# Kernel tuning notes

Hardware: AMD Instinct MI355X
Metric: run time of the kernel (lower is better)

## Reference

```python
import jax, jax.numpy as jnp
import numpy as np

NEG_SLOPE = 0.2
EPS = 1e-16


def _add_self_loops(edge_index, num_nodes):
    loop = jnp.arange(num_nodes, dtype=edge_index.dtype)
    return jnp.concatenate([edge_index, jnp.stack([loop, loop])], axis=1)


def gat_conv(x, edge_index, W, a_src, a_dst, b, concat):
    """PyG-style GATConv: gather -> attention logits -> segment softmax -> scatter-add."""
    N = x.shape[0]
    H, C = a_src.shape
    xl = (x @ W).reshape(N, H, C)                       # [N,H,C]
    alpha_src = (xl * a_src[None]).sum(-1)              # [N,H]
    alpha_dst = (xl * a_dst[None]).sum(-1)              # [N,H]
    src, dst = edge_index[0], edge_index[1]
    alpha = jax.nn.leaky_relu(alpha_src[src] + alpha_dst[dst], NEG_SLOPE)  # [E,H]
    amax = jax.ops.segment_max(alpha, dst, num_segments=N)
    amax = jnp.where(jnp.isfinite(amax), amax, 0.0)
    ea = jnp.exp(alpha - amax[dst])
    denom = jax.ops.segment_sum(ea, dst, num_segments=N)
    attn = ea / (denom[dst] + EPS)                      # [E,H]
    msg = xl[src] * attn[:, :, None]                    # [E,H,C]
    out = jax.ops.segment_sum(msg, dst, num_segments=N)  # [N,H,C]
    out = out.reshape(N, H * C) if concat else out.mean(axis=1)
    return out + b


def setup_inputs() -> dict:
    key = jax.random.key(0)
    ks = jax.random.split(key, 9)
    N, F, E, H, C, NC = 100000, 128, 1600000, 8, 8, 40
    s = lambda fan: 1.0 / np.sqrt(fan)
    return {
        "x": jax.random.normal(ks[0], (N, F), dtype=jnp.float32),
        "edge_index": jax.random.randint(ks[1], (2, E), 0, N, dtype=jnp.int64),
        "W1": jax.random.normal(ks[2], (F, H * C), dtype=jnp.float32) * s(F),
        "a_src1": jax.random.normal(ks[3], (H, C), dtype=jnp.float32) * s(C),
        "a_dst1": jax.random.normal(ks[4], (H, C), dtype=jnp.float32) * s(C),
        "b1": jnp.zeros((H * C,), dtype=jnp.float32),
        "W2": jax.random.normal(ks[5], (H * C, NC), dtype=jnp.float32) * s(H * C),
        "a_src2": jax.random.normal(ks[6], (1, NC), dtype=jnp.float32) * s(NC),
        "a_dst2": jax.random.normal(ks[7], (1, NC), dtype=jnp.float32) * s(NC),
        "b2": jnp.zeros((NC,), dtype=jnp.float32),
    }


def reference(x, edge_index, W1, a_src1, a_dst1, b1, W2, a_src2, a_dst2, b2):
    N = x.shape[0]
    ei = _add_self_loops(edge_index, N)
    h = gat_conv(x, ei, W1, a_src1, a_dst1, b1, concat=True)   # [N,64]
    h = jax.nn.elu(h)
    out = gat_conv(h, ei, W2, a_src2, a_dst2, b2, concat=True)  # [N,nclass]
    return out
```

## Files before the change

kernel.cpp:

```cpp
#include <hip/hip_runtime.h>
#include <math.h>

#define NEG_SLOPE 0.2f
#define GAT_EPS 1e-16f
#define LOG2E 1.44269504088896340736f

#define CH   8192
#define NBK  256

__device__ __forceinline__ unsigned pack_bf16(float a, float b) {
    unsigned ua = __float_as_uint(a);
    unsigned ub = __float_as_uint(b);
    ua = (ua + 0x8000u) >> 16;
    ub = (ub + 0x8000u) & 0xffff0000u;
    return ua | ub;
}
__device__ __forceinline__ float bf_lo(unsigned pk) {
    return __uint_as_float(pk << 16);
}
__device__ __forceinline__ float bf_hi(unsigned pk) {
    return __uint_as_float(pk & 0xffff0000u);
}


__global__ __launch_bounds__(256) void k_cnt(
    const int* __restrict__ ei, int E, int N, int shift,
    int* __restrict__ cnt)
{
    __shared__ int h[NBK];
    int c = blockIdx.x;
    h[threadIdx.x] = 0;
    __syncthreads();
    int Etot = E + N;
    int base = c * CH;
    int lim = min(base + CH, Etot);
    for (int e = base + threadIdx.x; e < lim; e += 256) {
        int d = (e < E) ? ei[E + e] : (e - E);
        atomicAdd(&h[d >> shift], 1);
    }
    __syncthreads();
    cnt[c * NBK + threadIdx.x] = h[threadIdx.x];
}

__global__ __launch_bounds__(256) void k_off_a(
    const int* __restrict__ cnt, int* __restrict__ off,
    int* __restrict__ tot, int NCH)
{
    __shared__ int sm[256];
    int b = blockIdx.x;
    int t = threadIdx.x;
    int carry = 0;
    for (int c0 = 0; c0 < NCH; c0 += 256) {
        int c = c0 + t;
        int v = (c < NCH) ? cnt[c * NBK + b] : 0;
        sm[t] = v;
        __syncthreads();
        for (int o = 1; o < 256; o <<= 1) {
            int add = (t >= o) ? sm[t - o] : 0;
            __syncthreads();
            sm[t] += add;
            __syncthreads();
        }
        if (c < NCH) off[c * NBK + b] = carry + sm[t] - v;
        carry += sm[255];
        __syncthreads();
    }
    if (t == 0) tot[b] = carry;
}

__global__ __launch_bounds__(256) void k_off_b(
    const int* __restrict__ tot, int* __restrict__ bbase)
{
    __shared__ int sm[NBK];
    int b = threadIdx.x;
    int v0 = tot[b];
    sm[b] = v0;
    __syncthreads();
    for (int o = 1; o < NBK; o <<= 1) {
        int v = (b >= o) ? sm[b - o] : 0;
        __syncthreads();
        sm[b] += v;
        __syncthreads();
    }
    bbase[b] = sm[b] - v0;
    if (b == NBK - 1) bbase[NBK] = sm[b];
}

__global__ __launch_bounds__(256) void k_place(
    const int* __restrict__ ei, int E, int N, int shift,
    const int* __restrict__ off, const int* __restrict__ bbase,
    unsigned* __restrict__ bslab)
{
    __shared__ int cur[NBK];
    int c = blockIdx.x;
    cur[threadIdx.x] = bbase[threadIdx.x] + off[c * NBK + threadIdx.x];
    __syncthreads();
    int Etot = E + N;
    int base = c * CH;
    int lim = min(base + CH, Etot);
    int mask = (1 << shift) - 1;
    for (int e = base + threadIdx.x; e < lim; e += 256) {
        int s, d;
        if (e < E) { s = ei[e]; d = ei[E + e]; }
        else       { s = e - E; d = s; }
        int b = d >> shift;
        int pos = atomicAdd(&cur[b], 1);
        bslab[pos] = (unsigned)s | ((unsigned)(d & mask) << 17);
    }
}

__global__ __launch_bounds__(256) void k_csr2(
    const int* __restrict__ bbase, const unsigned* __restrict__ bslab,
    int shift, int* __restrict__ row_ptr, int* __restrict__ csr_src,
    int N, int Etot)
{
    __shared__ int sdeg[1024];
    __shared__ int scur[1024];
    __shared__ int ps[256];
    int b = blockIdx.x;
    int tid = threadIdx.x;
    int beg = bbase[b], end = bbase[b + 1];
    int nodes = 1 << shift;
    int node0 = b << shift;
    for (int i = tid; i < nodes; i += 256) sdeg[i] = 0;
    __syncthreads();
    for (int i = beg + tid; i < end; i += 256)
        atomicAdd(&sdeg[bslab[i] >> 17], 1);
    __syncthreads();
    int per = (nodes + 255) / 256;
    int mybase = tid * per;
    int sum = 0;
    for (int j = 0; j < per; j++) sum += sdeg[mybase + j];
    ps[tid] = sum;
    __syncthreads();
    int v0 = ps[tid];
    for (int o = 1; o < 256; o <<= 1) {
        int v = (tid >= o) ? ps[tid - o] : 0;
        __syncthreads();
        ps[tid] += v;
        __syncthreads();
    }
    int run = ps[tid] - v0;
    for (int j = 0; j < per; j++) {
        int i = mybase + j;
        int dgi = sdeg[i];
        scur[i] = beg + run;
        int node = node0 + i;
        if (node < N) row_ptr[node] = beg + run;
        run += dgi;
    }
    if (b == 0 && tid == 0) row_ptr[N] = Etot;
    __syncthreads();
    for (int i = beg + tid; i < end; i += 256) {
        unsigned w = bslab[i];
        int pos = atomicAdd(&scur[w >> 17], 1);
        csr_src[pos] = (int)(w & 0x1FFFFu);
    }
}

__global__ __launch_bounds__(256) void k_gemm1(
    const float* __restrict__ x, const float* __restrict__ W1,
    const float* __restrict__ a_src1, const float* __restrict__ a_dst1,
    unsigned* __restrict__ xl1b, float* __restrict__ as1,
    float* __restrict__ ad1, int N, int F)
{
    __shared__ float Ws[128 * 64];
    __shared__ float asrc[64];
    __shared__ float adst[64];
    for (int i = threadIdx.x; i < F * 64; i += 256) Ws[i] = W1[i];
    if (threadIdx.x < 64) {
        asrc[threadIdx.x] = a_src1[threadIdx.x];
        adst[threadIdx.x] = a_dst1[threadIdx.x];
    }
    __syncthreads();

    int n = blockIdx.x * 64 + (threadIdx.x >> 2);
    int q = threadIdx.x & 3;
    if (n >= N) return;
    int c0 = q * 16;

    float acc[16];
#pragma unroll
    for (int c = 0; c < 16; c++) acc[c] = 0.0f;

    const float4* xr4 = (const float4*)(x + (size_t)n * F);
    for (int k4 = 0; k4 < F / 4; k4++) {
        float4 xv = xr4[k4];
        const float* w0 = &Ws[(k4 * 4 + 0) * 64 + c0];
        const float* w1 = &Ws[(k4 * 4 + 1) * 64 + c0];
        const float* w2 = &Ws[(k4 * 4 + 2) * 64 + c0];
        const float* w3 = &Ws[(k4 * 4 + 3) * 64 + c0];
#pragma unroll
        for (int c = 0; c < 16; c++) {
            float a = acc[c];
            a = fmaf(xv.x, w0[c], a);
            a = fmaf(xv.y, w1[c], a);
            a = fmaf(xv.z, w2[c], a);
            a = fmaf(xv.w, w3[c], a);
            acc[c] = a;
        }
    }

    uint4 pk0, pk1;
    pk0.x = pack_bf16(acc[0], acc[1]);  pk0.y = pack_bf16(acc[2], acc[3]);
    pk0.z = pack_bf16(acc[4], acc[5]);  pk0.w = pack_bf16(acc[6], acc[7]);
    pk1.x = pack_bf16(acc[8], acc[9]);  pk1.y = pack_bf16(acc[10], acc[11]);
    pk1.z = pack_bf16(acc[12], acc[13]); pk1.w = pack_bf16(acc[14], acc[15]);
    uint4* xo = (uint4*)(xl1b + (size_t)n * 32 + q * 8);
    xo[0] = pk0;
    xo[1] = pk1;

#pragma unroll
    for (int hh = 0; hh < 2; hh++) {
        float s = 0.0f, t = 0.0f;
#pragma unroll
        for (int c = 0; c < 8; c++) {
            s = fmaf(acc[hh * 8 + c], asrc[c0 + hh * 8 + c], s);
            t = fmaf(acc[hh * 8 + c], adst[c0 + hh * 8 + c], t);
        }
        as1[(size_t)n * 8 + 2 * q + hh] = s * LOG2E;
        ad1[(size_t)n * 8 + 2 * q + hh] = t * LOG2E;
    }
}

__global__ __launch_bounds__(256) void k_agg1(
    const int* __restrict__ row_ptr, const int* __restrict__ csr_src,
    const float* __restrict__ as1, const float* __restrict__ ad1,
    const unsigned* __restrict__ xl1b, const float* __restrict__ b1,
    float* __restrict__ h1, int N)
{
    int d = blockIdx.x * 8 + ((threadIdx.x >> 6) << 1) + ((threadIdx.x >> 5) & 1);
    if (d >= N) return;
    int lane = threadIdx.x & 31;
    int g = lane >> 3;
    int l = lane & 7;

    int beg = row_ptr[d], end = row_ptr[d + 1];
    float adh = ad1[(size_t)d * 8 + l];

    float ax[8];
#pragma unroll
    for (int j = 0; j < 8; j++) ax[j] = 0.f;
    float den = 0.f;

    int i = beg + g;
    for (; i + 4 < end; i += 8) {
        int s0 = csr_src[i];
        int s1 = csr_src[i + 4];
        size_t q0 = (size_t)s0 * 8 + l;
        size_t q1 = (size_t)s1 * 8 + l;
        float al0 = as1[q0] + adh;
        float al1 = as1[q1] + adh;
        uint4 k0 = *(const uint4*)(xl1b + (q0 << 2));
        uint4 k1 = *(const uint4*)(xl1b + (q1 << 2));
        al0 = fmaxf(al0, NEG_SLOPE * al0);
        al1 = fmaxf(al1, NEG_SLOPE * al1);
        float e0 = __builtin_amdgcn_exp2f(al0);
        float e1 = __builtin_amdgcn_exp2f(al1);
        ax[0] = fmaf(e0, bf_lo(k0.x), ax[0]);
        ax[1] = fmaf(e0, bf_hi(k0.x), ax[1]);
        ax[2] = fmaf(e0, bf_lo(k0.y), ax[2]);
        ax[3] = fmaf(e0, bf_hi(k0.y), ax[3]);
        ax[4] = fmaf(e0, bf_lo(k0.z), ax[4]);
        ax[5] = fmaf(e0, bf_hi(k0.z), ax[5]);
        ax[6] = fmaf(e0, bf_lo(k0.w), ax[6]);
        ax[7] = fmaf(e0, bf_hi(k0.w), ax[7]);
        ax[0] = fmaf(e1, bf_lo(k1.x), ax[0]);
        ax[1] = fmaf(e1, bf_hi(k1.x), ax[1]);
        ax[2] = fmaf(e1, bf_lo(k1.y), ax[2]);
        ax[3] = fmaf(e1, bf_hi(k1.y), ax[3]);
        ax[4] = fmaf(e1, bf_lo(k1.z), ax[4]);
        ax[5] = fmaf(e1, bf_hi(k1.z), ax[5]);
        ax[6] = fmaf(e1, bf_lo(k1.w), ax[6]);
        ax[7] = fmaf(e1, bf_hi(k1.w), ax[7]);
        den += e0 + e1;
    }
    if (i < end) {
        int s0 = csr_src[i];
        size_t q0 = (size_t)s0 * 8 + l;
        float al0 = as1[q0] + adh;
        uint4 k0 = *(const uint4*)(xl1b + (q0 << 2));
        al0 = fmaxf(al0, NEG_SLOPE * al0);
        float e0 = __builtin_amdgcn_exp2f(al0);
        ax[0] = fmaf(e0, bf_lo(k0.x), ax[0]);
        ax[1] = fmaf(e0, bf_hi(k0.x), ax[1]);
        ax[2] = fmaf(e0, bf_lo(k0.y), ax[2]);
        ax[3] = fmaf(e0, bf_hi(k0.y), ax[3]);
        ax[4] = fmaf(e0, bf_lo(k0.z), ax[4]);
        ax[5] = fmaf(e0, bf_hi(k0.z), ax[5]);
        ax[6] = fmaf(e0, bf_lo(k0.w), ax[6]);
        ax[7] = fmaf(e0, bf_hi(k0.w), ax[7]);
        den += e0;
    }

#pragma unroll
    for (int m = 8; m < 32; m <<= 1) {
#pragma unroll
        for (int j = 0; j < 8; j++) ax[j] += __shfl_xor(ax[j], m);
        den += __shfl_xor(den, m);
    }

    if (g == 0) {
        float inv = __builtin_amdgcn_rcpf(den + GAT_EPS);
        const float4* bb = (const float4*)(b1 + l * 8);
        float4 b0 = bb[0], b1v = bb[1];
        float4 o0, o1;
        float v;
        v = fmaf(ax[0], inv, b0.x);  o0.x = v > 0.f ? v : __expf(v) - 1.f;
        v = fmaf(ax[1], inv, b0.y);  o0.y = v > 0.f ? v : __expf(v) - 1.f;
        v = fmaf(ax[2], inv, b0.z);  o0.z = v > 0.f ? v : __expf(v) - 1.f;
        v = fmaf(ax[3], inv, b0.w);  o0.w = v > 0.f ? v : __expf(v) - 1.f;
        v = fmaf(ax[4], inv, b1v.x); o1.x = v > 0.f ? v : __expf(v) - 1.f;
        v = fmaf(ax[5], inv, b1v.y); o1.y = v > 0.f ? v : __expf(v) - 1.f;
        v = fmaf(ax[6], inv, b1v.z); o1.z = v > 0.f ? v : __expf(v) - 1.f;
        v = fmaf(ax[7], inv, b1v.w); o1.w = v > 0.f ? v : __expf(v) - 1.f;
        float4* op = (float4*)(h1 + (size_t)d * 64 + l * 8);
        op[0] = o0;
        op[1] = o1;
    }
}

__global__ __launch_bounds__(256) void k_node2(
    const float* __restrict__ h1, const float* __restrict__ W2,
    const float* __restrict__ a_src2, const float* __restrict__ a_dst2,
    unsigned* __restrict__ xl2b, float* __restrict__ as2,
    float* __restrict__ ad2, int N)
{
    __shared__ float Ws[64 * 40];
    __shared__ float a2s[40];
    __shared__ float a2d[40];
    for (int i = threadIdx.x; i < 64 * 40; i += 256) Ws[i] = W2[i];
    if (threadIdx.x < 40) {
        a2s[threadIdx.x] = a_src2[threadIdx.x];
        a2d[threadIdx.x] = a_dst2[threadIdx.x];
    }
    __syncthreads();

    int n = blockIdx.x * 128 + (threadIdx.x >> 1);
    int q = threadIdx.x & 1;
    if (n >= N) return;
    int c0 = q * 20;

    float o[20];
#pragma unroll
    for (int j = 0; j < 20; j++) o[j] = 0.0f;

    const float4* hr4 = (const float4*)(h1 + (size_t)n * 64);
    for (int k4 = 0; k4 < 16; k4++) {
        float4 hv = hr4[k4];
        const float* w0 = &Ws[(k4 * 4 + 0) * 40 + c0];
        const float* w1 = &Ws[(k4 * 4 + 1) * 40 + c0];
        const float* w2 = &Ws[(k4 * 4 + 2) * 40 + c0];
        const float* w3 = &Ws[(k4 * 4 + 3) * 40 + c0];
#pragma unroll
        for (int j = 0; j < 20; j++) {
            float a = o[j];
            a = fmaf(hv.x, w0[j], a);
            a = fmaf(hv.y, w1[j], a);
            a = fmaf(hv.z, w2[j], a);
            a = fmaf(hv.w, w3[j], a);
            o[j] = a;
        }
    }

    float s = 0.0f, t = 0.0f;
#pragma unroll
    for (int j = 0; j < 20; j++) {
        s = fmaf(o[j], a2s[c0 + j], s);
        t = fmaf(o[j], a2d[c0 + j], t);
    }
    s += __shfl_xor(s, 1);
    t += __shfl_xor(t, 1);
    if (q == 0) { as2[n] = s * LOG2E; ad2[n] = t * LOG2E; }

    unsigned* xo = xl2b + (size_t)n * 20 + q * 10;
#pragma unroll
    for (int p = 0; p < 10; p++) xo[p] = pack_bf16(o[2 * p], o[2 * p + 1]);
}

__global__ __launch_bounds__(256) void k_agg2(
    const int* __restrict__ row_ptr, const int* __restrict__ csr_src,
    const float* __restrict__ as2, const float* __restrict__ ad2,
    const unsigned* __restrict__ xl2b, const float* __restrict__ b2,
    float* __restrict__ out, int N)
{
    int d = blockIdx.x * 8 + ((threadIdx.x >> 6) << 1) + ((threadIdx.x >> 5) & 1);
    if (d >= N) return;
    int lane = threadIdx.x & 31;
    int g = lane >> 3;
    int l = lane & 7;
    if (l >= 5) return;

    int beg = row_ptr[d], end = row_ptr[d + 1];
    float add = ad2[d];

    float ax[8];
#pragma unroll
    for (int j = 0; j < 8; j++) ax[j] = 0.f;
    float den = 0.f;

    int i = beg + g;
    for (; i + 4 < end; i += 8) {
        int s0 = csr_src[i];
        int s1 = csr_src[i + 4];
        float al0 = as2[s0] + add;
        float al1 = as2[s1] + add;
        uint4 k0 = *(const uint4*)(xl2b + (size_t)s0 * 20 + l * 4);
        uint4 k1 = *(const uint4*)(xl2b + (size_t)s1 * 20 + l * 4);
        al0 = fmaxf(al0, NEG_SLOPE * al0);
        al1 = fmaxf(al1, NEG_SLOPE * al1);
        float e0 = __builtin_amdgcn_exp2f(al0);
        float e1 = __builtin_amdgcn_exp2f(al1);
        ax[0] = fmaf(e0, bf_lo(k0.x), ax[0]);
        ax[1] = fmaf(e0, bf_hi(k0.x), ax[1]);
        ax[2] = fmaf(e0, bf_lo(k0.y), ax[2]);
        ax[3] = fmaf(e0, bf_hi(k0.y), ax[3]);
        ax[4] = fmaf(e0, bf_lo(k0.z), ax[4]);
        ax[5] = fmaf(e0, bf_hi(k0.z), ax[5]);
        ax[6] = fmaf(e0, bf_lo(k0.w), ax[6]);
        ax[7] = fmaf(e0, bf_hi(k0.w), ax[7]);
        ax[0] = fmaf(e1, bf_lo(k1.x), ax[0]);
        ax[1] = fmaf(e1, bf_hi(k1.x), ax[1]);
        ax[2] = fmaf(e1, bf_lo(k1.y), ax[2]);
        ax[3] = fmaf(e1, bf_hi(k1.y), ax[3]);
        ax[4] = fmaf(e1, bf_lo(k1.z), ax[4]);
        ax[5] = fmaf(e1, bf_hi(k1.z), ax[5]);
        ax[6] = fmaf(e1, bf_lo(k1.w), ax[6]);
        ax[7] = fmaf(e1, bf_hi(k1.w), ax[7]);
        den += e0 + e1;
    }
    if (i < end) {
        int s0 = csr_src[i];
        float al0 = as2[s0] + add;
        uint4 k0 = *(const uint4*)(xl2b + (size_t)s0 * 20 + l * 4);
        al0 = fmaxf(al0, NEG_SLOPE * al0);
        float e0 = __builtin_amdgcn_exp2f(al0);
        ax[0] = fmaf(e0, bf_lo(k0.x), ax[0]);
        ax[1] = fmaf(e0, bf_hi(k0.x), ax[1]);
        ax[2] = fmaf(e0, bf_lo(k0.y), ax[2]);
        ax[3] = fmaf(e0, bf_hi(k0.y), ax[3]);
        ax[4] = fmaf(e0, bf_lo(k0.z), ax[4]);
        ax[5] = fmaf(e0, bf_hi(k0.z), ax[5]);
        ax[6] = fmaf(e0, bf_lo(k0.w), ax[6]);
        ax[7] = fmaf(e0, bf_hi(k0.w), ax[7]);
        den += e0;
    }

#pragma unroll
    for (int m = 8; m < 32; m <<= 1) {
#pragma unroll
        for (int j = 0; j < 8; j++) ax[j] += __shfl_xor(ax[j], m);
        den += __shfl_xor(den, m);
    }

    if (g == 0) {
        float inv = __builtin_amdgcn_rcpf(den + GAT_EPS);
        float* op = out + (size_t)d * 40 + l * 8;
        const float* bb = b2 + l * 8;
#pragma unroll
        for (int j = 0; j < 8; j++) op[j] = fmaf(ax[j], inv, bb[j]);
    }
}

extern "C" void kernel_launch(void* const* d_in, const int* in_sizes, int n_in,
                              void* d_out, int out_size, void* d_ws, size_t ws_size,
                              hipStream_t stream) {
    const float* x      = (const float*)d_in[0];
    const int*   ei     = (const int*)d_in[1];
    const float* W1     = (const float*)d_in[2];
    const float* a_src1 = (const float*)d_in[3];
    const float* a_dst1 = (const float*)d_in[4];
    const float* b1     = (const float*)d_in[5];
    const float* W2     = (const float*)d_in[6];
    const float* a_src2 = (const float*)d_in[7];
    const float* a_dst2 = (const float*)d_in[8];
    const float* b2     = (const float*)d_in[9];

    int F = in_sizes[2] / 64;
    int N = in_sizes[0] / F;
    int E = in_sizes[1] / 2;
    int Etot = E + N;
    int NCH = (Etot + CH - 1) / CH;
    int shift = 9;
    while (((N - 1) >> shift) >= NBK) shift++;

    unsigned* xl1b    = (unsigned*)d_ws;
    float*    h1      = (float*)(xl1b + (size_t)N * 32);
    float*    as1     = h1 + (size_t)N * 64;
    float*    ad1     = as1 + (size_t)N * 8;
    int*      row_ptr = (int*)(ad1 + (size_t)N * 8);
    int*      csr_src = row_ptr + (N + 1);
    int*      cnt     = csr_src + Etot;
    int*      off     = cnt + (size_t)NCH * NBK;
    int*      tot     = off + (size_t)NCH * NBK;
    int*      bbase   = tot + NBK;
    unsigned* bslab   = (unsigned*)(bbase + NBK + 1);
    unsigned* xl2b    = xl1b;
    float*    as2     = as1;
    float*    ad2     = ad1;

    k_cnt  <<<NCH, 256, 0, stream>>>(ei, E, N, shift, cnt);
    k_off_a<<<NBK, 256, 0, stream>>>(cnt, off, tot, NCH);
    k_off_b<<<1, 256, 0, stream>>>(tot, bbase);
    k_place<<<NCH, 256, 0, stream>>>(ei, E, N, shift, off, bbase, bslab);
    k_csr2 <<<NBK, 256, 0, stream>>>(bbase, bslab, shift,
                                     row_ptr, csr_src, N, Etot);

    k_gemm1<<<(N + 63) / 64, 256, 0, stream>>>(x, W1, a_src1, a_dst1,
                                               xl1b, as1, ad1, N, F);
    k_agg1 <<<(N + 7) / 8, 256, 0, stream>>>(row_ptr, csr_src, as1, ad1,
                                             xl1b, b1, h1, N);

    k_node2<<<(N + 127) / 128, 256, 0, stream>>>(h1, W2, a_src2, a_dst2,
                                                 xl2b, as2, ad2, N);
    k_agg2 <<<(N + 7) / 8, 256, 0, stream>>>(row_ptr, csr_src, as2, ad2,
                                             xl2b, b2, (float*)d_out, N);
}
```

Baseline: 299.1 us.

## Fuse CSR histogram into gemm1, drop offset kernels, pack layer-2 logits into rows

The per-chunk destination histogram moves into the first GEMM kernel, so it runs in extra or shared blocks of that launch. The two prefix-scan kernels are removed: the place and CSR kernels now recompute bucket offsets directly from the count array. The layer-2 source attention logit is stored inside each padded 24-word xl2b row, so the aggregation gathers one row per edge instead of two arrays. This cuts kernel launches and scattered loads, at the cost of redundant prefix work in every place/CSR block and a larger per-row stride.

```diff
diff --git a/kernel.cpp b/kernel.cpp
--- a/kernel.cpp
+++ b/kernel.cpp
@@ -23,78 +23,32 @@
 }
 
 
-__global__ __launch_bounds__(256) void k_cnt(
-    const int* __restrict__ ei, int E, int N, int shift,
-    int* __restrict__ cnt)
-{
-    __shared__ int h[NBK];
-    int c = blockIdx.x;
-    h[threadIdx.x] = 0;
-    __syncthreads();
-    int Etot = E + N;
-    int base = c * CH;
-    int lim = min(base + CH, Etot);
-    for (int e = base + threadIdx.x; e < lim; e += 256) {
-        int d = (e < E) ? ei[E + e] : (e - E);
-        atomicAdd(&h[d >> shift], 1);
-    }
-    __syncthreads();
-    cnt[c * NBK + threadIdx.x] = h[threadIdx.x];
-}
-
-__global__ __launch_bounds__(256) void k_off_a(
-    const int* __restrict__ cnt, int* __restrict__ off,
-    int* __restrict__ tot, int NCH)
-{
-    __shared__ int sm[256];
-    int b = blockIdx.x;
-    int t = threadIdx.x;
-    int carry = 0;
-    for (int c0 = 0; c0 < NCH; c0 += 256) {
-        int c = c0 + t;
-        int v = (c < NCH) ? cnt[c * NBK + b] : 0;
-        sm[t] = v;
-        __syncthreads();
-        for (int o = 1; o < 256; o <<= 1) {
-            int add = (t >= o) ? sm[t - o] : 0;
-            __syncthreads();
-            sm[t] += add;
-            __syncthreads();
-        }
-        if (c < NCH) off[c * NBK + b] = carry + sm[t] - v;
-        carry += sm[255];
-        __syncthreads();
-    }
-    if (t == 0) tot[b] = carry;
-}
-
-__global__ __launch_bounds__(256) void k_off_b(
-    const int* __restrict__ tot, int* __restrict__ bbase)
-{
-    __shared__ int sm[NBK];
-    int b = threadIdx.x;
-    int v0 = tot[b];
-    sm[b] = v0;
-    __syncthreads();
-    for (int o = 1; o < NBK; o <<= 1) {
-        int v = (b >= o) ? sm[b - o] : 0;
-        __syncthreads();
-        sm[b] += v;
-        __syncthreads();
-    }
-    bbase[b] = sm[b] - v0;
-    if (b == NBK - 1) bbase[NBK] = sm[b];
-}
-
 __global__ __launch_bounds__(256) void k_place(
     const int* __restrict__ ei, int E, int N, int shift,
-    const int* __restrict__ off, const int* __restrict__ bbase,
+    const int* __restrict__ cnt, int NCHv,
     unsigned* __restrict__ bslab)
 {
     __shared__ int cur[NBK];
+    __shared__ int cs[NBK];
     int c = blockIdx.x;
-    cur[threadIdx.x] = bbase[threadIdx.x] + off[c * NBK + threadIdx.x];
-    __syncthreads();
+    int t = threadIdx.x;
+    int pre = 0, tot = 0;
+    for (int cc = 0; cc < NCHv; cc++) {
+        int v = cnt[cc * NBK + t];
+        tot += v;
+        if (cc < c) pre += v;
+    }
+    cs[t] = tot;
+    __syncthreads();
+    for (int o = 1; o < 256; o <<= 1) {
+        int v = (t >= o) ? cs[t - o] : 0;
+        __syncthreads();
+        cs[t] += v;
+        __syncthreads();
+    }
+    cur[t] = (cs[t] - tot) + pre;
+    __syncthreads();
+
     int Etot = E + N;
     int base = c * CH;
     int lim = min(base + CH, Etot);
@@ -110,16 +64,33 @@
 }
 
 __global__ __launch_bounds__(256) void k_csr2(
-    const int* __restrict__ bbase, const unsigned* __restrict__ bslab,
+    const int* __restrict__ cnt, int NCHv,
+    const unsigned* __restrict__ bslab,
     int shift, int* __restrict__ row_ptr, int* __restrict__ csr_src,
     int N, int Etot)
 {
     __shared__ int sdeg[1024];
     __shared__ int scur[1024];
     __shared__ int ps[256];
+    __shared__ int bbs[NBK + 1];
     int b = blockIdx.x;
     int tid = threadIdx.x;
-    int beg = bbase[b], end = bbase[b + 1];
+
+    int tot = 0;
+    for (int cc = 0; cc < NCHv; cc++) tot += cnt[cc * NBK + tid];
+    ps[tid] = tot;
+    __syncthreads();
+    for (int o = 1; o < 256; o <<= 1) {
+        int v = (tid >= o) ? ps[tid - o] : 0;
+        __syncthreads();
+        ps[tid] += v;
+        __syncthreads();
+    }
+    bbs[tid] = ps[tid] - tot;
+    if (tid == 255) bbs[256] = ps[255];
+    __syncthreads();
+
+    int beg = bbs[b], end = bbs[b + 1];
     int nodes = 1 << shift;
     int node0 = b << shift;
     for (int i = tid; i < nodes; i += 256) sdeg[i] = 0;
@@ -162,11 +133,29 @@
     const float* __restrict__ x, const float* __restrict__ W1,
     const float* __restrict__ a_src1, const float* __restrict__ a_dst1,
     unsigned* __restrict__ xl1b, float* __restrict__ as1,
-    float* __restrict__ ad1, int N, int F)
+    float* __restrict__ ad1, int N, int F,
+    const int* __restrict__ ei, int E, int shift, int NCHv,
+    int* __restrict__ cnt)
 {
     __shared__ float Ws[128 * 64];
     __shared__ float asrc[64];
     __shared__ float adst[64];
+    __shared__ int hist[NBK];
+
+    if (blockIdx.x < NCHv) {
+        hist[threadIdx.x] = 0;
+        __syncthreads();
+        int Etot = E + N;
+        int base = blockIdx.x * CH;
+        int lim = min(base + CH, Etot);
+        for (int e = base + threadIdx.x; e < lim; e += 256) {
+            int d = (e < E) ? ei[E + e] : (e - E);
+            atomicAdd(&hist[d >> shift], 1);
+        }
+        __syncthreads();
+        cnt[blockIdx.x * NBK + threadIdx.x] = hist[threadIdx.x];
+    }
+
     for (int i = threadIdx.x; i < F * 64; i += 256) Ws[i] = W1[i];
     if (threadIdx.x < 64) {
         asrc[threadIdx.x] = a_src1[threadIdx.x];
@@ -323,8 +312,7 @@
 __global__ __launch_bounds__(256) void k_node2(
     const float* __restrict__ h1, const float* __restrict__ W2,
     const float* __restrict__ a_src2, const float* __restrict__ a_dst2,
-    unsigned* __restrict__ xl2b, float* __restrict__ as2,
-    float* __restrict__ ad2, int N)
+    unsigned* __restrict__ xl2b, float* __restrict__ ad2, int N)
 {
     __shared__ float Ws[64 * 40];
     __shared__ float a2s[40];
@@ -371,16 +359,19 @@
     }
     s += __shfl_xor(s, 1);
     t += __shfl_xor(t, 1);
-    if (q == 0) { as2[n] = s * LOG2E; ad2[n] = t * LOG2E; }
-
-    unsigned* xo = xl2b + (size_t)n * 20 + q * 10;
+    if (q == 0) {
+        xl2b[(size_t)n * 24 + 20] = __float_as_uint(s * LOG2E);
+        ad2[n] = t * LOG2E;
+    }
+
+    unsigned* xo = xl2b + (size_t)n * 24 + q * 10;
 #pragma unroll
     for (int p = 0; p < 10; p++) xo[p] = pack_bf16(o[2 * p], o[2 * p + 1]);
 }
 
 __global__ __launch_bounds__(256) void k_agg2(
     const int* __restrict__ row_ptr, const int* __restrict__ csr_src,
-    const float* __restrict__ as2, const float* __restrict__ ad2,
+    const float* __restrict__ ad2,
     const unsigned* __restrict__ xl2b, const float* __restrict__ b2,
     float* __restrict__ out, int N)
 {
@@ -403,10 +394,12 @@
     for (; i + 4 < end; i += 8) {
         int s0 = csr_src[i];
         int s1 = csr_src[i + 4];
-        float al0 = as2[s0] + add;
-        float al1 = as2[s1] + add;
-        uint4 k0 = *(const uint4*)(xl2b + (size_t)s0 * 20 + l * 4);
-        uint4 k1 = *(const uint4*)(xl2b + (size_t)s1 * 20 + l * 4);
+        const unsigned* r0 = xl2b + (size_t)s0 * 24;
+        const unsigned* r1 = xl2b + (size_t)s1 * 24;
+        float al0 = __uint_as_float(r0[20]) + add;
+        float al1 = __uint_as_float(r1[20]) + add;
+        uint4 k0 = *(const uint4*)(r0 + l * 4);
+        uint4 k1 = *(const uint4*)(r1 + l * 4);
         al0 = fmaxf(al0, NEG_SLOPE * al0);
         al1 = fmaxf(al1, NEG_SLOPE * al1);
         float e0 = __builtin_amdgcn_exp2f(al0);
@@ -431,8 +424,9 @@
     }
     if (i < end) {
         int s0 = csr_src[i];
-        float al0 = as2[s0] + add;
-        uint4 k0 = *(const uint4*)(xl2b + (size_t)s0 * 20 + l * 4);
+        const unsigned* r0 = xl2b + (size_t)s0 * 24;
+        float al0 = __uint_as_float(r0[20]) + add;
+        uint4 k0 = *(const uint4*)(r0 + l * 4);
         al0 = fmaxf(al0, NEG_SLOPE * al0);
         float e0 = __builtin_amdgcn_exp2f(al0);
         ax[0] = fmaf(e0, bf_lo(k0.x), ax[0]);
@@ -480,7 +474,7 @@
     int N = in_sizes[0] / F;
     int E = in_sizes[1] / 2;
     int Etot = E + N;
-    int NCH = (Etot + CH - 1) / CH;
+    int NCHv = (Etot + CH - 1) / CH;
     int shift = 9;
     while (((N - 1) >> shift) >= NBK) shift++;
 
@@ -491,28 +485,25 @@
     int*      row_ptr = (int*)(ad1 + (size_t)N * 8);
     int*      csr_src = row_ptr + (N + 1);
     int*      cnt     = csr_src + Etot;
-    int*      off     = cnt + (size_t)NCH * NBK;
-    int*      tot     = off + (size_t)NCH * NBK;
-    int*      bbase   = tot + NBK;
-    unsigned* bslab   = (unsigned*)(bbase + NBK + 1);
+    unsigned* bslab   = (unsigned*)(cnt + (size_t)NCHv * NBK);
     unsigned* xl2b    = xl1b;
-    float*    as2     = as1;
     float*    ad2     = ad1;
 
-    k_cnt  <<<NCH, 256, 0, stream>>>(ei, E, N, shift, cnt);
-    k_off_a<<<NBK, 256, 0, stream>>>(cnt, off, tot, NCH);
-    k_off_b<<<1, 256, 0, stream>>>(tot, bbase);
-    k_place<<<NCH, 256, 0, stream>>>(ei, E, N, shift, off, bbase, bslab);
-    k_csr2 <<<NBK, 256, 0, stream>>>(bbase, bslab, shift,
+    int gridG1 = (N + 63) / 64;
+    if (gridG1 < NCHv) gridG1 = NCHv;
+    k_gemm1<<<gridG1, 256, 0, stream>>>(x, W1, a_src1, a_dst1,
+                                        xl1b, as1, ad1, N, F,
+                                        ei, E, shift, NCHv, cnt);
+
+    k_place<<<NCHv, 256, 0, stream>>>(ei, E, N, shift, cnt, NCHv, bslab);
+    k_csr2 <<<NBK, 256, 0, stream>>>(cnt, NCHv, bslab, shift,
                                      row_ptr, csr_src, N, Etot);
 
-    k_gemm1<<<(N + 63) / 64, 256, 0, stream>>>(x, W1, a_src1, a_dst1,
-                                               xl1b, as1, ad1, N, F);
     k_agg1 <<<(N + 7) / 8, 256, 0, stream>>>(row_ptr, csr_src, as1, ad1,
                                              xl1b, b1, h1, N);
 
     k_node2<<<(N + 127) / 128, 256, 0, stream>>>(h1, W2, a_src2, a_dst2,
-                                                 xl2b, as2, ad2, N);
-    k_agg2 <<<(N + 7) / 8, 256, 0, stream>>>(row_ptr, csr_src, as2, ad2,
+                                                 xl2b, ad2, N);
+    k_agg2 <<<(N + 7) / 8, 256, 0, stream>>>(row_ptr, csr_src, ad2,
                                              xl2b, b2, (float*)d_out, N);
 }
```

Result: slower. 335.2 us (+12.1%).
